# Optimization experiments

Measured on AMD Instinct MI355X. Metric: run time of the kernel, lower is better.

## Reference

```python
import jax, jax.numpy as jnp
import numpy as np


def setup_inputs() -> dict:
    B, K, E, M, H, T, V = 32, 64, 512, 512, 512, 20, 32000
    key = jax.random.key(0)
    ks = jax.random.split(key, 8)
    s = 0.02
    return {
        "encoder_outputs": jax.random.normal(ks[0], (B, K, E), jnp.float32),
        "embedding_table": jax.random.normal(ks[1], (V, M), jnp.float32) * s,
        "Wa": jax.random.normal(ks[2], (2 * H + E, 1), jnp.float32) * s,
        "ba": jnp.zeros((1,), jnp.float32),
        "W_ih": jax.random.normal(ks[3], (4 * H, E + M), jnp.float32) * s,
        "W_hh": jax.random.normal(ks[4], (4 * H, H), jnp.float32) * s,
        "b_ih": jnp.zeros((4 * H,), jnp.float32),
        "b_hh": jnp.zeros((4 * H,), jnp.float32),
        "Wl": jax.random.normal(ks[5], (V, 2 * H + E + M), jnp.float32) * s,
        "bl": jnp.zeros((V,), jnp.float32),
        "captions": jax.random.randint(ks[6], (B, T), 0, V),
        "use_teacher_forcing": 1,
    }


def reference(encoder_outputs, embedding_table, Wa, ba, W_ih, W_hh, b_ih, b_hh,
              Wl, bl, captions, use_teacher_forcing):
    B, K, E = encoder_outputs.shape
    H = W_hh.shape[1]
    tf = bool(use_teacher_forcing)  # static python flag

    # h0 = c0 = last encoder output (requires E == H, as in the source)
    h0 = encoder_outputs[:, -1, :]
    c0 = h0

    caps_seq = captions.T  # (T, B); captions[:, i] becomes next token after step i

    def step(carry, cap_t):
        h, c, token = carry
        emb = embedding_table[token]                       # (B, M), dropout=0
        flat_state = jnp.concatenate([h, c], axis=-1)      # (B, 2H)
        # Bahdanau alignment over all K encoder steps at once
        al_in = jnp.concatenate(
            [jnp.broadcast_to(flat_state[:, None, :], (B, K, 2 * H)),
             encoder_outputs], axis=-1)                    # (B, K, 2H+E)
        scores = jnp.tanh(al_in @ Wa + ba)[..., 0]         # (B, K)
        attn = jax.nn.softmax(scores, axis=1)
        context = jnp.einsum('bk,bke->be', attn, encoder_outputs)  # (B, E)
        x = jnp.concatenate([context, emb], axis=-1)       # (B, E+M) == rnn_input
        # single LSTM step, PyTorch gate order i,f,g,o
        gates = x @ W_ih.T + b_ih + h @ W_hh.T + b_hh
        i_g, f_g, g_g, o_g = jnp.split(gates, 4, axis=-1)
        c_new = jax.nn.sigmoid(f_g) * c + jax.nn.sigmoid(i_g) * jnp.tanh(g_g)
        h_new = jax.nn.sigmoid(o_g) * jnp.tanh(c_new)
        # NOTE: source concatenates the PRE-update state here (faithful)
        final_input = jnp.concatenate([flat_state, x], axis=-1)  # (B, 2H+E+M)
        logp = jax.nn.log_softmax(final_input @ Wl.T + bl, axis=1)  # (B, V)
        next_token = cap_t if tf else jnp.argmax(logp, axis=1)
        return (h_new, c_new, next_token), logp

    init = (h0, c0, captions[:, 0])
    _, probs = jax.lax.scan(step, init, caps_seq)
    return jnp.transpose(probs, (1, 0, 2))  # (B, T, V)
```

## Files before the change

### kernel.cpp

```cpp
#include <hip/hip_runtime.h>
#include <hip/hip_bf16.h>
#include <stdint.h>

#define B_   32
#define K_   64
#define E_   512
#define H_   512
#define M_   512
#define T_   20
#define V_   32000
#define KIN  2048
#define NBLK 32

typedef __bf16 bf16x8 __attribute__((ext_vector_type(8)));
typedef float  f32x4  __attribute__((ext_vector_type(4)));

__device__ inline unsigned short f2bf_rne(float f) {
  union { float f; unsigned u; } v; v.f = f;
  unsigned r = v.u + 0x7FFFu + ((v.u >> 16) & 1u);
  return (unsigned short)(r >> 16);
}
__device__ inline float bf2f(unsigned short s) {
  union { unsigned u; float f; } v; v.u = ((unsigned)s) << 16;
  return v.f;
}
__device__ inline float sigm(float x) { return 1.f / (1.f + expf(-x)); }
__device__ inline unsigned ordf(float f) {
  unsigned u = __float_as_uint(f);
  return (u & 0x80000000u) ? ~u : (u | 0x80000000u);
}
__device__ __forceinline__ void gload16(const void* g, void* l) {
  __builtin_amdgcn_global_load_lds(
      (const __attribute__((address_space(1))) void*)g,
      (__attribute__((address_space(3))) void*)l, 16, 0, 0);
}


__global__ void k_prep(const float* __restrict__ W_ih, const float* __restrict__ W_hh,
                       const float* __restrict__ b_ih, const float* __restrict__ b_hh,
                       const float* __restrict__ enc, const float* __restrict__ embt,
                       const int* __restrict__ captions,
                       unsigned short* __restrict__ wih_hi, unsigned short* __restrict__ wih_lo,
                       unsigned short* __restrict__ whh_hi, unsigned short* __restrict__ whh_lo,
                       unsigned short* __restrict__ enc_bf, unsigned short* __restrict__ emb_bf,
                       float* __restrict__ bias_arr, float* __restrict__ score_part,
                       unsigned long long* __restrict__ argkey) {
  int tid0 = blockIdx.x * 256 + threadIdx.x;
  int NT = gridDim.x * 256;
  for (int i = tid0; i < 2048 * 1024; i += NT) {
    float f = W_ih[i];
    unsigned short h = f2bf_rne(f);
    wih_hi[i] = h; wih_lo[i] = f2bf_rne(f - bf2f(h));
  }
  for (int i = tid0; i < NBLK * 64 * 512; i += NT) {
    int e = i & 511, jj = (i >> 9) & 63, blk = i >> 15;
    int jg = (jj >> 4) * 512 + blk * 16 + (jj & 15);
    float f = W_hh[jg * 512 + e];
    unsigned short h = f2bf_rne(f);
    whh_hi[i] = h; whh_lo[i] = f2bf_rne(f - bf2f(h));
  }
  for (int i = tid0; i < 2048 * 512; i += NT) enc_bf[i] = f2bf_rne(enc[i]);
  for (int i = tid0; i < 640 * 512; i += NT) {
    int n = i >> 9, m = i & 511;
    int t = n >> 5, b = n & 31;
    int tok = captions[b * T_ + (t > 0 ? t - 1 : 0)];
    emb_bf[i] = f2bf_rne(embt[(size_t)tok * 512 + m]);
  }
  for (int i = tid0; i < 2048; i += NT) {
    int blk = i >> 6, jj = i & 63;
    int jg = (jj >> 4) * 512 + blk * 16 + (jj & 15);
    bias_arr[i] = b_ih[jg] + b_hh[jg];
  }
  for (int i = tid0; i < (T_ + 1) * 1024; i += NT) score_part[i] = 0.f;
  for (int i = tid0; i < 32; i += NT) argkey[i] = 0ull;
}

__global__ void k_init(const float* __restrict__ enc, const float* __restrict__ Wa,
                       float* __restrict__ hb, float* __restrict__ cb,
                       unsigned short* __restrict__ Fall,
                       float* __restrict__ enc_score, float* __restrict__ score_part) {
  int idx = blockIdx.x * 256 + threadIdx.x;
  int b = idx >> 9, i = idx & 511;
  float v = enc[(size_t)b * K_ * E_ + (size_t)(K_ - 1) * E_ + i];
  hb[b * H_ + i] = v;
  cb[b * H_ + i] = v;
  unsigned short bv = f2bf_rne(v);
  Fall[b * KIN + i] = bv;
  Fall[b * KIN + H_ + i] = bv;
  if (idx < B_ * K_) {
    int bb = idx >> 6, k = idx & 63;
    const float4* e4  = (const float4*)(enc + ((size_t)bb * K_ + k) * E_);
    const float4* wa4 = (const float4*)(Wa + 2 * H_);
    float acc = 0.f;
    #pragma unroll 4
    for (int q = 0; q < E_ / 4; ++q) {
      float4 a = e4[q], w = wa4[q];
      acc += a.x * w.x + a.y * w.y + a.z * w.z + a.w * w.w;
    }
    enc_score[idx] = acc;
  }
  if (idx < 2048) {
    int bb = idx >> 6, l = idx & 63;
    float s = 0.f;
    #pragma unroll
    for (int q = 0; q < 8; ++q) {
      int ii = l * 8 + q;
      float hv = enc[(size_t)bb * K_ * E_ + (size_t)(K_ - 1) * E_ + ii];
      s += hv * (Wa[ii] + Wa[512 + ii]);
    }
    for (int o = 32; o; o >>= 1) s += __shfl_down(s, o);
    if (l == 0) score_part[bb] = s;
  }
}

__global__ __launch_bounds__(256) void k_gpre(
    const unsigned short* __restrict__ whi, const unsigned short* __restrict__ wlo,
    int koff, const unsigned short* __restrict__ Bm,
    float* __restrict__ outp, int N) {
  int blk = blockIdx.x, nt = blockIdx.y;
  int tid = threadIdx.x;
  int l = tid & 63, w = tid >> 6, lv = l & 15, lg = l >> 4;
  const int n0 = nt * 128 + w * 32;

  f32x4 acc[4][2];
  #pragma unroll
  for (int jf = 0; jf < 4; ++jf)
    #pragma unroll
    for (int nf = 0; nf < 2; ++nf) acc[jf][nf] = (f32x4){0.f, 0.f, 0.f, 0.f};

  #pragma unroll 4
  for (int kk = 0; kk < 16; ++kk) {
    bf16x8 bfr[2];
    #pragma unroll
    for (int nf = 0; nf < 2; ++nf)
      bfr[nf] = *(const bf16x8*)(Bm + (size_t)(n0 + nf * 16 + lv) * 512 + kk * 32 + lg * 8);
    #pragma unroll
    for (int jf = 0; jf < 4; ++jf) {
      int jg = jf * 512 + blk * 16 + lv;
      bf16x8 ahi = *(const bf16x8*)(whi + (size_t)jg * 1024 + koff + kk * 32 + lg * 8);
      bf16x8 alo = *(const bf16x8*)(wlo + (size_t)jg * 1024 + koff + kk * 32 + lg * 8);
      #pragma unroll
      for (int nf = 0; nf < 2; ++nf) {
        acc[jf][nf] = __builtin_amdgcn_mfma_f32_16x16x32_bf16(ahi, bfr[nf], acc[jf][nf], 0, 0, 0);
        acc[jf][nf] = __builtin_amdgcn_mfma_f32_16x16x32_bf16(alo, bfr[nf], acc[jf][nf], 0, 0, 0);
      }
    }
  }
  #pragma unroll
  for (int jf = 0; jf < 4; ++jf)
    #pragma unroll
    for (int nf = 0; nf < 2; ++nf)
      #pragma unroll
      for (int jr = 0; jr < 4; ++jr) {
        int n = n0 + nf * 16 + lv;
        int jj = jf * 16 + 4 * lg + jr;
        outp[((size_t)blk * N + n) * 64 + jj] = acc[jf][nf][jr];
      }
}

__global__ __launch_bounds__(256) void k_step(
    const float* __restrict__ enc, const float* __restrict__ embt,
    const float* __restrict__ Wa, const float* __restrict__ ba,
    const float* __restrict__ W_ih, const float* __restrict__ W_hh,
    const float* __restrict__ b_ih, const float* __restrict__ b_hh,
    const float* __restrict__ Wl, const float* __restrict__ bl,
    const int* __restrict__ captions, const int* __restrict__ tf_flag,
    const float* __restrict__ Genc, const float* __restrict__ Gemb,
    const unsigned short* __restrict__ whh_hi, const unsigned short* __restrict__ whh_lo,
    const float* __restrict__ bias_arr, const float* __restrict__ enc_score,
    float* __restrict__ score_part, float* __restrict__ attn_w,
    unsigned short* __restrict__ Fall, float* __restrict__ hb, float* __restrict__ cb,
    unsigned long long* __restrict__ argkey, int t) {
  const int blk = blockIdx.x;
  const int tid = threadIdx.x;
  __shared__ float attn_s[B_ * K_];
  __shared__ float gsA[64 * 33];
  __shared__ float scC[512];
  __shared__ float score_t[32];
  const float* cbc = cb + (t & 1) * B_ * H_;
  float* cbn = cb + ((t + 1) & 1) * B_ * H_;

  if (tf_flag[0]) {
    if (tid < 32) {
      float s = 0.f;
      #pragma unroll 8
      for (int p = 0; p < 32; ++p) s += score_part[t * 1024 + p * 32 + tid];
      score_t[tid] = s;
    }
    __syncthreads();
    {
      int w = tid >> 6, l = tid & 63;
      float ba0 = ba[0];
      for (int bb = 0; bb < 8; ++bb) {
        int b = w * 8 + bb;
        float s = tanhf(score_t[b] + enc_score[b * 64 + l] + ba0);
        float m = s;
        for (int o = 32; o; o >>= 1) m = fmaxf(m, __shfl_xor(m, o));
        float e = expf(s - m);
        float sum = e;
        for (int o = 32; o; o >>= 1) sum += __shfl_xor(sum, o);
        float a = e / sum;
        attn_s[b * 64 + l] = a;
        if (b == blk) attn_w[(t * 32 + b) * 64 + l] = a;
      }
    }
    __syncthreads();
    {
      const f32x4* G4 = (const f32x4*)Genc;
      const f32x4* E4 = (const f32x4*)Gemb;
      const f32x4* B4 = (const f32x4*)bias_arr;
      #pragma unroll
      for (int rr = 0; rr < 2; ++rr) {
        int idx = rr * 256 + tid;
        int b = idx >> 4, jj4 = idx & 15;
        const f32x4* gp = G4 + ((size_t)blk * 2048 + b * 64) * 16 + jj4;
        const float* ap = attn_s + b * 64;
        f32x4 s = {0.f, 0.f, 0.f, 0.f};
        #pragma unroll 8
        for (int k = 0; k < 64; ++k) {
          float a = ap[k];
          f32x4 g = gp[(size_t)k * 16];
          s[0] += a * g[0]; s[1] += a * g[1]; s[2] += a * g[2]; s[3] += a * g[3];
        }
        f32x4 e = E4[((size_t)blk * 640 + t * 32 + b) * 16 + jj4];
        f32x4 bb = B4[blk * 16 + jj4];
        #pragma unroll
        for (int q = 0; q < 4; ++q) {
          float v = s[q] + (e[q] + bb[q]);
          gsA[(jj4 * 4 + q) * 33 + b] = v;
        }
      }
    }
    __syncthreads();
    {
      int g = tid >> 6, l = tid & 63, lv = l & 15, lg = l >> 4;
      const unsigned short* ah = whh_hi + ((size_t)blk * 64 + g * 16 + lv) * 512 + lg * 8;
      const unsigned short* al = whh_lo + ((size_t)blk * 64 + g * 16 + lv) * 512 + lg * 8;
      const unsigned short* f0 = Fall + ((size_t)t * 32 + lv) * KIN + lg * 8;
      const unsigned short* f1 = Fall + ((size_t)t * 32 + 16 + lv) * KIN + lg * 8;
      f32x4 a0 = {0.f, 0.f, 0.f, 0.f};
      f32x4 a1 = {0.f, 0.f, 0.f, 0.f};
      #pragma unroll 8
      for (int kk = 0; kk < 16; ++kk) {
        bf16x8 hi = *(const bf16x8*)(ah + kk * 32);
        bf16x8 lo = *(const bf16x8*)(al + kk * 32);
        bf16x8 b0 = *(const bf16x8*)(f0 + kk * 32);
        bf16x8 b1 = *(const bf16x8*)(f1 + kk * 32);
        a0 = __builtin_amdgcn_mfma_f32_16x16x32_bf16(hi, b0, a0, 0, 0, 0);
        a0 = __builtin_amdgcn_mfma_f32_16x16x32_bf16(lo, b0, a0, 0, 0, 0);
        a1 = __builtin_amdgcn_mfma_f32_16x16x32_bf16(hi, b1, a1, 0, 0, 0);
        a1 = __builtin_amdgcn_mfma_f32_16x16x32_bf16(lo, b1, a1, 0, 0, 0);
      }
      #pragma unroll
      for (int jr = 0; jr < 4; ++jr) {
        int jj = g * 16 + 4 * lg + jr;
        gsA[jj * 33 + lv]      += a0[jr];
        gsA[jj * 33 + 16 + lv] += a1[jr];
      }
    }
    __syncthreads();
    #pragma unroll
    for (int rr = 0; rr < 2; ++rr) {
      int idx = tid + rr * 256;
      int b = idx & 31, r = idx >> 5;
      int ii = blk * 16 + r;
      float ig = gsA[(r) * 33 + b];
      float fg = gsA[(16 + r) * 33 + b];
      float gg = gsA[(32 + r) * 33 + b];
      float og = gsA[(48 + r) * 33 + b];
      float cv = cbc[b * H_ + ii];
      float cn = sigm(fg) * cv + sigm(ig) * tanhf(gg);
      float hn = sigm(og) * tanhf(cn);
      cbn[b * H_ + ii] = cn;
      Fall[((size_t)(t + 1) * 32 + b) * KIN + ii] = f2bf_rne(hn);
      Fall[((size_t)(t + 1) * 32 + b) * KIN + H_ + ii] = f2bf_rne(cn);
      scC[r * 32 + b] = hn * Wa[ii] + cn * Wa[512 + ii];
    }
    __syncthreads();
    if (tid < 32) {
      float s = 0.f;
      #pragma unroll
      for (int r = 0; r < 16; ++r) s += scC[r * 32 + tid];
      score_part[(t + 1) * 1024 + blk * 32 + tid] = s;
    }
  } else {
    const int b = blk;
    __shared__ float xls[KIN];
    __shared__ float gls[2048];
    __shared__ int tok_s;
    __shared__ unsigned long long bred[256];
    const float* hbc = hb + (t & 1) * B_ * H_;
    float* hbn = hb + ((t + 1) & 1) * B_ * H_;
    if (tid == 0) {
      float s = 0.f;
      for (int p = 0; p < 32; ++p) s += score_part[t * 1024 + p * 32 + b];
      score_t[0] = s;
      tok_s = (t == 0) ? captions[b * T_]
                       : (int)(0xFFFFFFFFu - (unsigned)(argkey[b] & 0xFFFFFFFFull));
    }
    __syncthreads();
    if (tid < 64) {
      float s = tanhf(score_t[0] + enc_score[b * 64 + tid] + ba[0]);
      float m = s;
      for (int o = 32; o; o >>= 1) m = fmaxf(m, __shfl_xor(m, o));
      float e = expf(s - m);
      float sum = e;
      for (int o = 32; o; o >>= 1) sum += __shfl_xor(sum, o);
      attn_s[tid] = e / sum;
    }
    __syncthreads();
    for (int i = tid; i < 512; i += 256) {
      xls[i] = hbc[b * H_ + i];
      xls[512 + i] = cbc[b * H_ + i];
      float a = 0.f;
      for (int k = 0; k < 64; ++k) a += attn_s[k] * enc[((size_t)b * 64 + k) * 512 + i];
      xls[1024 + i] = a;
      xls[1536 + i] = embt[(size_t)tok_s * 512 + i];
    }
    __syncthreads();
    for (int i = tid; i < 1024; i += 256)
      Fall[((size_t)t * 32 + b) * KIN + 1024 + i] = f2bf_rne(xls[1024 + i]);
    for (int j = tid; j < 2048; j += 256) {
      float a = b_ih[j] + b_hh[j];
      for (int e = 0; e < 1024; ++e) a += W_ih[(size_t)j * 1024 + e] * xls[1024 + e];
      for (int e = 0; e < 512; ++e)  a += W_hh[(size_t)j * 512 + e] * xls[e];
      gls[j] = a;
    }
    __syncthreads();
    {
      float sc = 0.f;
      for (int i = tid; i < 512; i += 256) {
        float ig = gls[i], fg = gls[512 + i], gg = gls[1024 + i], og = gls[1536 + i];
        float cv = xls[512 + i];
        float cn = sigm(fg) * cv + sigm(ig) * tanhf(gg);
        float hn = sigm(og) * tanhf(cn);
        hbn[b * H_ + i] = hn;
        cbn[b * H_ + i] = cn;
        Fall[((size_t)(t + 1) * 32 + b) * KIN + i] = f2bf_rne(hn);
        Fall[((size_t)(t + 1) * 32 + b) * KIN + H_ + i] = f2bf_rne(cn);
        sc += hn * Wa[i] + cn * Wa[512 + i];
      }
      scC[tid] = sc;
    }
    __syncthreads();
    if (tid == 0) {
      float s = 0.f;
      for (int q = 0; q < 256; ++q) s += scC[q];
      score_part[(t + 1) * 1024 + b] = s;
    }
    unsigned long long best = 0ull;
    for (int v = tid; v < V_; v += 256) {
      float d = bl[v];
      const float* wr = Wl + (size_t)v * KIN;
      for (int k = 0; k < KIN; ++k) d += wr[k] * xls[k];
      unsigned long long key = ((unsigned long long)ordf(d) << 32) | (0xFFFFFFFFu - (unsigned)v);
      if (key > best) best = key;
    }
    bred[tid] = best;
    __syncthreads();
    for (int o = 128; o; o >>= 1) {
      if (tid < o) bred[tid] = bred[tid] > bred[tid + o] ? bred[tid] : bred[tid + o];
      __syncthreads();
    }
    if (tid == 0) argkey[b] = bred[0];
  }
}

__global__ void k_fill(const float* __restrict__ enc, const unsigned short* __restrict__ emb_bf,
                       const float* __restrict__ attn_w, const int* __restrict__ tf_flag,
                       unsigned short* __restrict__ Fall) {
  if (tf_flag[0] == 0) return;
  int n = blockIdx.x;
  int b = n & 31;
  int tid = threadIdx.x;
  __shared__ float aw[64];
  if (tid < 64) aw[tid] = attn_w[n * 64 + tid];
  __syncthreads();
  for (int e = tid; e < 512; e += 256) {
    float a = 0.f;
    #pragma unroll 8
    for (int k = 0; k < 64; ++k) a += aw[k] * enc[((size_t)b * 64 + k) * 512 + e];
    Fall[(size_t)n * KIN + 1024 + e] = f2bf_rne(a);
  }
  for (int m = tid; m < 512; m += 256)
    Fall[(size_t)n * KIN + 1536 + m] = emb_bf[n * 512 + m];
}

__global__ void k_conv(const float* __restrict__ src, unsigned short* __restrict__ dst, int n4) {
  int i = blockIdx.x * blockDim.x + threadIdx.x;
  int stride = gridDim.x * blockDim.x;
  for (; i < n4; i += stride) {
    f32x4 v = __builtin_nontemporal_load((const f32x4*)src + i);
    ushort4 o;
    o.x = f2bf_rne(v.x); o.y = f2bf_rne(v.y); o.z = f2bf_rne(v.z); o.w = f2bf_rne(v.w);
    ((ushort4*)dst)[i] = o;
  }
}

#define GM   128
#define GNP  320
#define ABYTES 40960
#define BUFB  57344

__global__ __launch_bounds__(512, 2) void k_gemm(
    const unsigned short* __restrict__ wl_bf,
    const unsigned short* __restrict__ F,
    const float* __restrict__ bl,
    float* __restrict__ out) {
  extern __shared__ unsigned char lds[];
  const int tid = threadIdx.x;
  const int l = tid & 63, w = tid >> 6, lv = l & 15, lg = l >> 4;
  const int wm = w >> 2, wn = w & 3;
  const int m0 = blockIdx.x * GM;

  float blv[4];
  #pragma unroll
  for (int mi = 0; mi < 4; ++mi) blv[mi] = bl[m0 + wm * 64 + mi * 16 + lv];

  f32x4 acc[4][5];
  #pragma unroll
  for (int mi = 0; mi < 4; ++mi)
    #pragma unroll
    for (int ni = 0; ni < 5; ++ni) acc[mi][ni] = (f32x4){0.f, 0.f, 0.f, 0.f};

#define STAGE(c, buf) do {                                                    \
    int kb_ = ((c) & 31) * 64;                                                \
    int nb_ = ((c) >> 5) * GNP;                                               \
    unsigned char* bs_ = lds + (buf) * BUFB;                                  \
    _Pragma("unroll")                                                         \
    for (int i_ = 0; i_ < 5; ++i_) {                                          \
      int s_ = i_ * 512 + tid;                                                \
      int kq_ = s_ / 320, n_ = s_ - kq_ * 320;                                \
      gload16(F + (size_t)(nb_ + n_) * KIN + kb_ + kq_ * 8, bs_ + s_ * 16);   \
    }                                                                         \
    _Pragma("unroll")                                                         \
    for (int j_ = 0; j_ < 2; ++j_) {                                          \
      int s_ = j_ * 512 + tid;                                                \
      int kq_ = s_ >> 7, m_ = s_ & 127;                                       \
      gload16(wl_bf + (size_t)(m0 + m_) * KIN + kb_ + kq_ * 8,                \
              bs_ + ABYTES + s_ * 16);                                        \
    }                                                                         \
  } while (0)

#define COMPUTE(buf) do {                                                     \
    unsigned char* bs_ = lds + (buf) * BUFB;                                  \
    _Pragma("unroll")                                                         \
    for (int kk2_ = 0; kk2_ < 2; ++kk2_) {                                    \
      int kq_ = kk2_ * 4 + lg;                                                \
      bf16x8 bf_[4];                                                          \
      _Pragma("unroll")                                                       \
      for (int mi = 0; mi < 4; ++mi)                                          \
        bf_[mi] = *(const bf16x8*)(bs_ + ABYTES +                             \
                    (size_t)(kq_ * 128 + wm * 64 + mi * 16 + lv) * 16);       \
      _Pragma("unroll")                                                       \
      for (int ni = 0; ni < 5; ++ni) {                                        \
        bf16x8 af_ = *(const bf16x8*)(bs_ +                                   \
                    (size_t)(kq_ * 320 + wn * 80 + ni * 16 + lv) * 16);       \
        _Pragma("unroll")                                                     \
        for (int mi = 0; mi < 4; ++mi)                                        \
          acc[mi][ni] = __builtin_amdgcn_mfma_f32_16x16x32_bf16(              \
                          af_, bf_[mi], acc[mi][ni], 0, 0, 0);                \
      }                                                                       \
    }                                                                         \
  } while (0)

#define WRITEOUT(pass) do {                                                   \
    _Pragma("unroll")                                                         \
    for (int mi = 0; mi < 4; ++mi) {                                          \
      int v_ = m0 + wm * 64 + mi * 16 + lv;                                   \
      _Pragma("unroll")                                                       \
      for (int ni = 0; ni < 5; ++ni) {                                        \
        _Pragma("unroll")                                                     \
        for (int j_ = 0; j_ < 4; ++j_) {                                      \
          int n_ = (pass) * GNP + wn * 80 + ni * 16 + 4 * lg + j_;            \
          int tt_ = n_ >> 5, bb_ = n_ & 31;                                   \
          out[((size_t)bb_ * T_ + tt_) * V_ + v_] = acc[mi][ni][j_] + blv[mi];\
        }                                                                     \
      }                                                                       \
    }                                                                         \
  } while (0)

  STAGE(0, 0);
  int cur = 0;
  for (int c = 0; c < 64; ++c) {
    __syncthreads();
    if (c < 63) STAGE(c + 1, cur ^ 1);
    COMPUTE(cur);
    if (c == 31) {
      WRITEOUT(0);
      #pragma unroll
      for (int mi = 0; mi < 4; ++mi)
        #pragma unroll
        for (int ni = 0; ni < 5; ++ni) acc[mi][ni] = (f32x4){0.f, 0.f, 0.f, 0.f};
    }
    cur ^= 1;
  }
  WRITEOUT(1);
#undef STAGE
#undef COMPUTE
#undef WRITEOUT
}

__global__ void k_lsm(float* __restrict__ out) {
  float4* p = (float4*)(out + (size_t)blockIdx.x * V_);
  int tid = threadIdx.x;
  __shared__ float smax[4], ssum[4];
  const int N4 = V_ / 4;
  float m = -1e30f, s = 0.f;
  for (int i = tid; i < N4; i += 256) {
    float4 v = p[i];
    float lm = fmaxf(fmaxf(v.x, v.y), fmaxf(v.z, v.w));
    if (lm > m) { s *= expf(m - lm); m = lm; }
    s += expf(v.x - m) + expf(v.y - m) + expf(v.z - m) + expf(v.w - m);
  }
  for (int o = 32; o; o >>= 1) {
    float m2 = __shfl_xor(m, o), s2 = __shfl_xor(s, o);
    float mn = fmaxf(m, m2);
    s = s * expf(m - mn) + s2 * expf(m2 - mn);
    m = mn;
  }
  if ((tid & 63) == 0) { smax[tid >> 6] = m; ssum[tid >> 6] = s; }
  __syncthreads();
  float mg = fmaxf(fmaxf(smax[0], smax[1]), fmaxf(smax[2], smax[3]));
  float sg = ssum[0] * expf(smax[0] - mg) + ssum[1] * expf(smax[1] - mg)
           + ssum[2] * expf(smax[2] - mg) + ssum[3] * expf(smax[3] - mg);
  float lse = mg + logf(sg);
  for (int i = tid; i < N4; i += 256) {
    float4 v = p[i];
    v.x -= lse; v.y -= lse; v.z -= lse; v.w -= lse;
    p[i] = v;
  }
}

extern "C" void kernel_launch(void* const* d_in, const int* in_sizes, int n_in,
                              void* d_out, int out_size, void* d_ws, size_t ws_size,
                              hipStream_t stream) {
  const float* enc      = (const float*)d_in[0];
  const float* embt     = (const float*)d_in[1];
  const float* Wa       = (const float*)d_in[2];
  const float* ba       = (const float*)d_in[3];
  const float* W_ih     = (const float*)d_in[4];
  const float* W_hh     = (const float*)d_in[5];
  const float* b_ih     = (const float*)d_in[6];
  const float* b_hh     = (const float*)d_in[7];
  const float* Wl       = (const float*)d_in[8];
  const float* bl       = (const float*)d_in[9];
  const int*   captions = (const int*)d_in[10];
  const int*   tf       = (const int*)d_in[11];
  float* out = (float*)d_out;
  char*  ws  = (char*)d_ws;

  size_t off = 0;
  unsigned short* Fall = (unsigned short*)(ws + off); off += (size_t)(T_ + 1) * B_ * KIN * 2;
  float* hb            = (float*)(ws + off);          off += (size_t)2 * B_ * H_ * 4;
  float* cb            = (float*)(ws + off);          off += (size_t)2 * B_ * H_ * 4;
  float* enc_score     = (float*)(ws + off);          off += (size_t)B_ * K_ * 4;
  float* score_part    = (float*)(ws + off);          off += (size_t)(T_ + 1) * 1024 * 4;
  float* attn_w        = (float*)(ws + off);          off += (size_t)T_ * B_ * K_ * 4;
  unsigned long long* argkey = (unsigned long long*)(ws + off); off += 256;
  float* bias_arr      = (float*)(ws + off);          off += 2048 * 4;
  off = (off + 1023) & ~(size_t)1023;
  unsigned short* wih_hi = (unsigned short*)(ws + off); off += (size_t)2048 * 1024 * 2;
  unsigned short* wih_lo = (unsigned short*)(ws + off); off += (size_t)2048 * 1024 * 2;
  unsigned short* whh_hi = (unsigned short*)(ws + off); off += (size_t)NBLK * 64 * 512 * 2;
  unsigned short* whh_lo = (unsigned short*)(ws + off); off += (size_t)NBLK * 64 * 512 * 2;
  unsigned short* enc_bf = (unsigned short*)(ws + off); off += (size_t)2048 * 512 * 2;
  unsigned short* emb_bf = (unsigned short*)(ws + off); off += (size_t)640 * 512 * 2;
  float* Genc          = (float*)(ws + off);          off += (size_t)NBLK * 2048 * 64 * 4;
  float* Gemb          = (float*)(ws + off);          off += (size_t)NBLK * 640 * 64 * 4;
  unsigned short* wl_bf = (unsigned short*)(ws + off); off += (size_t)V_ * KIN * 2;

  k_prep<<<512, 256, 0, stream>>>(W_ih, W_hh, b_ih, b_hh, enc, embt, captions,
                                  wih_hi, wih_lo, whh_hi, whh_lo, enc_bf, emb_bf,
                                  bias_arr, score_part, argkey);
  k_init<<<64, 256, 0, stream>>>(enc, Wa, hb, cb, Fall, enc_score, score_part);
  k_gpre<<<dim3(NBLK, 16), 256, 0, stream>>>(wih_hi, wih_lo, 0, enc_bf, Genc, 2048);
  k_gpre<<<dim3(NBLK, 5), 256, 0, stream>>>(wih_hi, wih_lo, 512, emb_bf, Gemb, 640);

  for (int t = 0; t < T_; ++t) {
    k_step<<<NBLK, 256, 0, stream>>>(enc, embt, Wa, ba, W_ih, W_hh, b_ih, b_hh,
                                     Wl, bl, captions, tf, Genc, Gemb,
                                     whh_hi, whh_lo, bias_arr, enc_score,
                                     score_part, attn_w, Fall, hb, cb, argkey, t);
  }
  k_fill<<<T_ * B_, 256, 0, stream>>>(enc, emb_bf, attn_w, tf, Fall);
  k_conv<<<8192, 256, 0, stream>>>(Wl, wl_bf, V_ * KIN / 4);
  k_gemm<<<V_ / GM, 512, 2 * BUFB, stream>>>(wl_bf, Fall, bl, out);
  k_lsm<<<B_ * T_, 256, 0, stream>>>(out);
}
```

Before: 813.4 us.

## Fuse per-step launches into one cooperative kernel and fold fill/conv into prep

Replaces the 20 per-timestep k_step launches with a single cooperative kernel that loops over timesteps and uses grid.sync between steps. The context-vector write to Fall now happens inside the step loop, removing k_fill and the attn_w buffer. The Wl-to-bf16 conversion and the embedding copy into Fall move into k_prep, removing the separate k_conv launch. This trades per-launch overhead for grid-wide barrier cost, and makes k_prep heavier.

```diff
diff --git a/kernel.cpp b/kernel.cpp
--- a/kernel.cpp
+++ b/kernel.cpp
@@ -1,6 +1,9 @@
 #include <hip/hip_runtime.h>
 #include <hip/hip_bf16.h>
+#include <hip/hip_cooperative_groups.h>
 #include <stdint.h>
+
+namespace cg = cooperative_groups;
 
 #define B_   32
 #define K_   64
@@ -44,9 +47,17 @@
                        unsigned short* __restrict__ whh_hi, unsigned short* __restrict__ whh_lo,
                        unsigned short* __restrict__ enc_bf, unsigned short* __restrict__ emb_bf,
                        float* __restrict__ bias_arr, float* __restrict__ score_part,
-                       unsigned long long* __restrict__ argkey) {
+                       unsigned long long* __restrict__ argkey,
+                       const float* __restrict__ Wl, unsigned short* __restrict__ wl_bf,
+                       unsigned short* __restrict__ Fall) {
   int tid0 = blockIdx.x * 256 + threadIdx.x;
   int NT = gridDim.x * 256;
+  for (int i = tid0; i < V_ * KIN / 4; i += NT) {
+    f32x4 v = __builtin_nontemporal_load((const f32x4*)Wl + i);
+    ushort4 o;
+    o.x = f2bf_rne(v.x); o.y = f2bf_rne(v.y); o.z = f2bf_rne(v.z); o.w = f2bf_rne(v.w);
+    ((ushort4*)wl_bf)[i] = o;
+  }
   for (int i = tid0; i < 2048 * 1024; i += NT) {
     float f = W_ih[i];
     unsigned short h = f2bf_rne(f);
@@ -64,7 +75,9 @@
     int n = i >> 9, m = i & 511;
     int t = n >> 5, b = n & 31;
     int tok = captions[b * T_ + (t > 0 ? t - 1 : 0)];
-    emb_bf[i] = f2bf_rne(embt[(size_t)tok * 512 + m]);
+    unsigned short ev = f2bf_rne(embt[(size_t)tok * 512 + m]);
+    emb_bf[i] = ev;
+    Fall[(size_t)n * KIN + 1536 + m] = ev;
   }
   for (int i = tid0; i < 2048; i += NT) {
     int blk = i >> 6, jj = i & 63;
@@ -158,7 +171,7 @@
       }
 }
 
-__global__ __launch_bounds__(256) void k_step(
+__global__ __launch_bounds__(256) void k_chain(
     const float* __restrict__ enc, const float* __restrict__ embt,
     const float* __restrict__ Wa, const float* __restrict__ ba,
     const float* __restrict__ W_ih, const float* __restrict__ W_hh,
@@ -168,232 +181,214 @@
     const float* __restrict__ Genc, const float* __restrict__ Gemb,
     const unsigned short* __restrict__ whh_hi, const unsigned short* __restrict__ whh_lo,
     const float* __restrict__ bias_arr, const float* __restrict__ enc_score,
-    float* __restrict__ score_part, float* __restrict__ attn_w,
-    unsigned short* __restrict__ Fall, float* __restrict__ hb, float* __restrict__ cb,
-    unsigned long long* __restrict__ argkey, int t) {
+    float* __restrict__ score_part, unsigned short* __restrict__ Fall,
+    float* __restrict__ hb, float* __restrict__ cb,
+    unsigned long long* __restrict__ argkey) {
+  cg::grid_group grid = cg::this_grid();
   const int blk = blockIdx.x;
   const int tid = threadIdx.x;
   __shared__ float attn_s[B_ * K_];
   __shared__ float gsA[64 * 33];
   __shared__ float scC[512];
-  __shared__ float score_t[32];
-  const float* cbc = cb + (t & 1) * B_ * H_;
-  float* cbn = cb + ((t + 1) & 1) * B_ * H_;
-
-  if (tf_flag[0]) {
-    if (tid < 32) {
-      float s = 0.f;
-      #pragma unroll 8
-      for (int p = 0; p < 32; ++p) s += score_part[t * 1024 + p * 32 + tid];
-      score_t[tid] = s;
-    }
-    __syncthreads();
-    {
-      int w = tid >> 6, l = tid & 63;
-      float ba0 = ba[0];
-      for (int bb = 0; bb < 8; ++bb) {
-        int b = w * 8 + bb;
-        float s = tanhf(score_t[b] + enc_score[b * 64 + l] + ba0);
+  __shared__ float score_t_[32];
+  __shared__ int   token_sp;
+  __shared__ float xls[KIN];
+  __shared__ float gls[2048];
+  __shared__ unsigned long long bred[256];
+  const int tf = tf_flag[0];
+
+  for (int t = 0; t < T_; ++t) {
+    const float* cbc = cb + (t & 1) * B_ * H_;
+    float* cbn = cb + ((t + 1) & 1) * B_ * H_;
+
+    if (tf) {
+      if (tid < 32) {
+        float s = 0.f;
+        #pragma unroll 8
+        for (int p = 0; p < 32; ++p) s += score_part[t * 1024 + p * 32 + tid];
+        score_t_[tid] = s;
+      }
+      __syncthreads();
+      {
+        int w = tid >> 6, l = tid & 63;
+        float ba0 = ba[0];
+        for (int bb = 0; bb < 8; ++bb) {
+          int b = w * 8 + bb;
+          float s = tanhf(score_t_[b] + enc_score[b * 64 + l] + ba0);
+          float m = s;
+          for (int o = 32; o; o >>= 1) m = fmaxf(m, __shfl_xor(m, o));
+          float e = expf(s - m);
+          float sum = e;
+          for (int o = 32; o; o >>= 1) sum += __shfl_xor(sum, o);
+          attn_s[b * 64 + l] = e / sum;
+        }
+      }
+      __syncthreads();
+      {
+        const f32x4* G4 = (const f32x4*)Genc;
+        const f32x4* E4 = (const f32x4*)Gemb;
+        const f32x4* B4 = (const f32x4*)bias_arr;
+        #pragma unroll
+        for (int rr = 0; rr < 2; ++rr) {
+          int idx = rr * 256 + tid;
+          int b = idx >> 4, jj4 = idx & 15;
+          const f32x4* gp = G4 + ((size_t)blk * 2048 + b * 64) * 16 + jj4;
+          const float* ap = attn_s + b * 64;
+          f32x4 s = {0.f, 0.f, 0.f, 0.f};
+          #pragma unroll 8
+          for (int k = 0; k < 64; ++k) {
+            float a = ap[k];
+            f32x4 g = gp[(size_t)k * 16];
+            s[0] += a * g[0]; s[1] += a * g[1]; s[2] += a * g[2]; s[3] += a * g[3];
+          }
+          f32x4 e = E4[((size_t)blk * 640 + t * 32 + b) * 16 + jj4];
+          f32x4 bb = B4[blk * 16 + jj4];
+          #pragma unroll
+          for (int q = 0; q < 4; ++q) {
+            float v = s[q] + (e[q] + bb[q]);
+            gsA[(jj4 * 4 + q) * 33 + b] = v;
+          }
+        }
+      }
+      {
+        const float* aw = attn_s + blk * 64;
+        for (int e = tid; e < 512; e += 256) {
+          float a = 0.f;
+          #pragma unroll 8
+          for (int k = 0; k < 64; ++k) a += aw[k] * enc[((size_t)blk * 64 + k) * 512 + e];
+          Fall[((size_t)t * 32 + blk) * KIN + 1024 + e] = f2bf_rne(a);
+        }
+      }
+      __syncthreads();
+      {
+        int g = tid >> 6, l = tid & 63, lv = l & 15, lg = l >> 4;
+        const unsigned short* ah = whh_hi + ((size_t)blk * 64 + g * 16 + lv) * 512 + lg * 8;
+        const unsigned short* al = whh_lo + ((size_t)blk * 64 + g * 16 + lv) * 512 + lg * 8;
+        const unsigned short* f0 = Fall + ((size_t)t * 32 + lv) * KIN + lg * 8;
+        const unsigned short* f1 = Fall + ((size_t)t * 32 + 16 + lv) * KIN + lg * 8;
+        f32x4 a0 = {0.f, 0.f, 0.f, 0.f};
+        f32x4 a1 = {0.f, 0.f, 0.f, 0.f};
+        #pragma unroll 8
+        for (int kk = 0; kk < 16; ++kk) {
+          bf16x8 hi = *(const bf16x8*)(ah + kk * 32);
+          bf16x8 lo = *(const bf16x8*)(al + kk * 32);
+          bf16x8 b0 = *(const bf16x8*)(f0 + kk * 32);
+          bf16x8 b1 = *(const bf16x8*)(f1 + kk * 32);
+          a0 = __builtin_amdgcn_mfma_f32_16x16x32_bf16(hi, b0, a0, 0, 0, 0);
+          a0 = __builtin_amdgcn_mfma_f32_16x16x32_bf16(lo, b0, a0, 0, 0, 0);
+          a1 = __builtin_amdgcn_mfma_f32_16x16x32_bf16(hi, b1, a1, 0, 0, 0);
+          a1 = __builtin_amdgcn_mfma_f32_16x16x32_bf16(lo, b1, a1, 0, 0, 0);
+        }
+        #pragma unroll
+        for (int jr = 0; jr < 4; ++jr) {
+          int jj = g * 16 + 4 * lg + jr;
+          gsA[jj * 33 + lv]      += a0[jr];
+          gsA[jj * 33 + 16 + lv] += a1[jr];
+        }
+      }
+      __syncthreads();
+      #pragma unroll
+      for (int rr = 0; rr < 2; ++rr) {
+        int idx = tid + rr * 256;
+        int b = idx & 31, r = idx >> 5;
+        int ii = blk * 16 + r;
+        float ig = gsA[(r) * 33 + b];
+        float fg = gsA[(16 + r) * 33 + b];
+        float gg = gsA[(32 + r) * 33 + b];
+        float og = gsA[(48 + r) * 33 + b];
+        float cv = cbc[b * H_ + ii];
+        float cn = sigm(fg) * cv + sigm(ig) * tanhf(gg);
+        float hn = sigm(og) * tanhf(cn);
+        cbn[b * H_ + ii] = cn;
+        Fall[((size_t)(t + 1) * 32 + b) * KIN + ii] = f2bf_rne(hn);
+        Fall[((size_t)(t + 1) * 32 + b) * KIN + H_ + ii] = f2bf_rne(cn);
+        scC[r * 32 + b] = hn * Wa[ii] + cn * Wa[512 + ii];
+      }
+      __syncthreads();
+      if (tid < 32) {
+        float s = 0.f;
+        #pragma unroll
+        for (int r = 0; r < 16; ++r) s += scC[r * 32 + tid];
+        score_part[(t + 1) * 1024 + blk * 32 + tid] = s;
+      }
+    } else {
+      const int b = blk;
+      const float* hbc = hb + (t & 1) * B_ * H_;
+      float* hbn = hb + ((t + 1) & 1) * B_ * H_;
+      if (tid == 0) {
+        float s = 0.f;
+        for (int p = 0; p < 32; ++p) s += score_part[t * 1024 + p * 32 + b];
+        score_t_[0] = s;
+        token_sp = (t == 0) ? captions[b * T_]
+                            : (int)(0xFFFFFFFFu - (unsigned)(argkey[b] & 0xFFFFFFFFull));
+      }
+      __syncthreads();
+      if (tid < 64) {
+        float s = tanhf(score_t_[0] + enc_score[b * 64 + tid] + ba[0]);
         float m = s;
         for (int o = 32; o; o >>= 1) m = fmaxf(m, __shfl_xor(m, o));
         float e = expf(s - m);
         float sum = e;
         for (int o = 32; o; o >>= 1) sum += __shfl_xor(sum, o);
-        float a = e / sum;
-        attn_s[b * 64 + l] = a;
-        if (b == blk) attn_w[(t * 32 + b) * 64 + l] = a;
-      }
+        attn_s[tid] = e / sum;
+      }
+      __syncthreads();
+      for (int i = tid; i < 512; i += 256) {
+        xls[i] = hbc[b * H_ + i];
+        xls[512 + i] = cbc[b * H_ + i];
+        float a = 0.f;
+        for (int k = 0; k < 64; ++k) a += attn_s[k] * enc[((size_t)b * 64 + k) * 512 + i];
+        xls[1024 + i] = a;
+        xls[1536 + i] = embt[(size_t)token_sp * 512 + i];
+      }
+      __syncthreads();
+      for (int i = tid; i < 1024; i += 256)
+        Fall[((size_t)t * 32 + b) * KIN + 1024 + i] = f2bf_rne(xls[1024 + i]);
+      for (int j = tid; j < 2048; j += 256) {
+        float a = b_ih[j] + b_hh[j];
+        for (int e = 0; e < 1024; ++e) a += W_ih[(size_t)j * 1024 + e] * xls[1024 + e];
+        for (int e = 0; e < 512; ++e)  a += W_hh[(size_t)j * 512 + e] * xls[e];
+        gls[j] = a;
+      }
+      __syncthreads();
+      {
+        float sc = 0.f;
+        for (int i = tid; i < 512; i += 256) {
+          float ig = gls[i], fg = gls[512 + i], gg = gls[1024 + i], og = gls[1536 + i];
+          float cv = xls[512 + i];
+          float cn = sigm(fg) * cv + sigm(ig) * tanhf(gg);
+          float hn = sigm(og) * tanhf(cn);
+          hbn[b * H_ + i] = hn;
+          cbn[b * H_ + i] = cn;
+          Fall[((size_t)(t + 1) * 32 + b) * KIN + i] = f2bf_rne(hn);
+          Fall[((size_t)(t + 1) * 32 + b) * KIN + H_ + i] = f2bf_rne(cn);
+          sc += hn * Wa[i] + cn * Wa[512 + i];
+        }
+        scC[tid] = sc;
+      }
+      __syncthreads();
+      if (tid == 0) {
+        float s = 0.f;
+        for (int q = 0; q < 256; ++q) s += scC[q];
+        score_part[(t + 1) * 1024 + b] = s;
+      }
+      unsigned long long best = 0ull;
+      for (int v = tid; v < V_; v += 256) {
+        float d = bl[v];
+        const float* wr = Wl + (size_t)v * KIN;
+        for (int k = 0; k < KIN; ++k) d += wr[k] * xls[k];
+        unsigned long long key = ((unsigned long long)ordf(d) << 32) | (0xFFFFFFFFu - (unsigned)v);
+        if (key > best) best = key;
+      }
+      bred[tid] = best;
+      __syncthreads();
+      for (int o = 128; o; o >>= 1) {
+        if (tid < o) bred[tid] = bred[tid] > bred[tid + o] ? bred[tid] : bred[tid + o];
+        __syncthreads();
+      }
+      if (tid == 0) argkey[b] = bred[0];
     }
-    __syncthreads();
-    {
-      const f32x4* G4 = (const f32x4*)Genc;
-      const f32x4* E4 = (const f32x4*)Gemb;
-      const f32x4* B4 = (const f32x4*)bias_arr;
-      #pragma unroll
-      for (int rr = 0; rr < 2; ++rr) {
-        int idx = rr * 256 + tid;
-        int b = idx >> 4, jj4 = idx & 15;
-        const f32x4* gp = G4 + ((size_t)blk * 2048 + b * 64) * 16 + jj4;
-        const float* ap = attn_s + b * 64;
-        f32x4 s = {0.f, 0.f, 0.f, 0.f};
-        #pragma unroll 8
-        for (int k = 0; k < 64; ++k) {
-          float a = ap[k];
-          f32x4 g = gp[(size_t)k * 16];
-          s[0] += a * g[0]; s[1] += a * g[1]; s[2] += a * g[2]; s[3] += a * g[3];
-        }
-        f32x4 e = E4[((size_t)blk * 640 + t * 32 + b) * 16 + jj4];
-        f32x4 bb = B4[blk * 16 + jj4];
-        #pragma unroll
-        for (int q = 0; q < 4; ++q) {
-          float v = s[q] + (e[q] + bb[q]);
-          gsA[(jj4 * 4 + q) * 33 + b] = v;
-        }
-      }
-    }
-    __syncthreads();
-    {
-      int g = tid >> 6, l = tid & 63, lv = l & 15, lg = l >> 4;
-      const unsigned short* ah = whh_hi + ((size_t)blk * 64 + g * 16 + lv) * 512 + lg * 8;
-      const unsigned short* al = whh_lo + ((size_t)blk * 64 + g * 16 + lv) * 512 + lg * 8;
-      const unsigned short* f0 = Fall + ((size_t)t * 32 + lv) * KIN + lg * 8;
-      const unsigned short* f1 = Fall + ((size_t)t * 32 + 16 + lv) * KIN + lg * 8;
-      f32x4 a0 = {0.f, 0.f, 0.f, 0.f};
-      f32x4 a1 = {0.f, 0.f, 0.f, 0.f};
-      #pragma unroll 8
-      for (int kk = 0; kk < 16; ++kk) {
-        bf16x8 hi = *(const bf16x8*)(ah + kk * 32);
-        bf16x8 lo = *(const bf16x8*)(al + kk * 32);
-        bf16x8 b0 = *(const bf16x8*)(f0 + kk * 32);
-        bf16x8 b1 = *(const bf16x8*)(f1 + kk * 32);
-        a0 = __builtin_amdgcn_mfma_f32_16x16x32_bf16(hi, b0, a0, 0, 0, 0);
-        a0 = __builtin_amdgcn_mfma_f32_16x16x32_bf16(lo, b0, a0, 0, 0, 0);
-        a1 = __builtin_amdgcn_mfma_f32_16x16x32_bf16(hi, b1, a1, 0, 0, 0);
-        a1 = __builtin_amdgcn_mfma_f32_16x16x32_bf16(lo, b1, a1, 0, 0, 0);
-      }
-      #pragma unroll
-      for (int jr = 0; jr < 4; ++jr) {
-        int jj = g * 16 + 4 * lg + jr;
-        gsA[jj * 33 + lv]      += a0[jr];
-        gsA[jj * 33 + 16 + lv] += a1[jr];
-      }
-    }
-    __syncthreads();
-    #pragma unroll
-    for (int rr = 0; rr < 2; ++rr) {
-      int idx = tid + rr * 256;
-      int b = idx & 31, r = idx >> 5;
-      int ii = blk * 16 + r;
-      float ig = gsA[(r) * 33 + b];
-      float fg = gsA[(16 + r) * 33 + b];
-      float gg = gsA[(32 + r) * 33 + b];
-      float og = gsA[(48 + r) * 33 + b];
-      float cv = cbc[b * H_ + ii];
-      float cn = sigm(fg) * cv + sigm(ig) * tanhf(gg);
-      float hn = sigm(og) * tanhf(cn);
-      cbn[b * H_ + ii] = cn;
-      Fall[((size_t)(t + 1) * 32 + b) * KIN + ii] = f2bf_rne(hn);
-      Fall[((size_t)(t + 1) * 32 + b) * KIN + H_ + ii] = f2bf_rne(cn);
-      scC[r * 32 + b] = hn * Wa[ii] + cn * Wa[512 + ii];
-    }
-    __syncthreads();
-    if (tid < 32) {
-      float s = 0.f;
-      #pragma unroll
-      for (int r = 0; r < 16; ++r) s += scC[r * 32 + tid];
-      score_part[(t + 1) * 1024 + blk * 32 + tid] = s;
-    }
-  } else {
-    const int b = blk;
-    __shared__ float xls[KIN];
-    __shared__ float gls[2048];
-    __shared__ int tok_s;
-    __shared__ unsigned long long bred[256];
-    const float* hbc = hb + (t & 1) * B_ * H_;
-    float* hbn = hb + ((t + 1) & 1) * B_ * H_;
-    if (tid == 0) {
-      float s = 0.f;
-      for (int p = 0; p < 32; ++p) s += score_part[t * 1024 + p * 32 + b];
-      score_t[0] = s;
-      tok_s = (t == 0) ? captions[b * T_]
-                       : (int)(0xFFFFFFFFu - (unsigned)(argkey[b] & 0xFFFFFFFFull));
-    }
-    __syncthreads();
-    if (tid < 64) {
-      float s = tanhf(score_t[0] + enc_score[b * 64 + tid] + ba[0]);
-      float m = s;
-      for (int o = 32; o; o >>= 1) m = fmaxf(m, __shfl_xor(m, o));
-      float e = expf(s - m);
-      float sum = e;
-      for (int o = 32; o; o >>= 1) sum += __shfl_xor(sum, o);
-      attn_s[tid] = e / sum;
-    }
-    __syncthreads();
-    for (int i = tid; i < 512; i += 256) {
-      xls[i] = hbc[b * H_ + i];
-      xls[512 + i] = cbc[b * H_ + i];
-      float a = 0.f;
-      for (int k = 0; k < 64; ++k) a += attn_s[k] * enc[((size_t)b * 64 + k) * 512 + i];
-      xls[1024 + i] = a;
-      xls[1536 + i] = embt[(size_t)tok_s * 512 + i];
-    }
-    __syncthreads();
-    for (int i = tid; i < 1024; i += 256)
-      Fall[((size_t)t * 32 + b) * KIN + 1024 + i] = f2bf_rne(xls[1024 + i]);
-    for (int j = tid; j < 2048; j += 256) {
-      float a = b_ih[j] + b_hh[j];
-      for (int e = 0; e < 1024; ++e) a += W_ih[(size_t)j * 1024 + e] * xls[1024 + e];
-      for (int e = 0; e < 512; ++e)  a += W_hh[(size_t)j * 512 + e] * xls[e];
-      gls[j] = a;
-    }
-    __syncthreads();
-    {
-      float sc = 0.f;
-      for (int i = tid; i < 512; i += 256) {
-        float ig = gls[i], fg = gls[512 + i], gg = gls[1024 + i], og = gls[1536 + i];
-        float cv = xls[512 + i];
-        float cn = sigm(fg) * cv + sigm(ig) * tanhf(gg);
-        float hn = sigm(og) * tanhf(cn);
-        hbn[b * H_ + i] = hn;
-        cbn[b * H_ + i] = cn;
-        Fall[((size_t)(t + 1) * 32 + b) * KIN + i] = f2bf_rne(hn);
-        Fall[((size_t)(t + 1) * 32 + b) * KIN + H_ + i] = f2bf_rne(cn);
-        sc += hn * Wa[i] + cn * Wa[512 + i];
-      }
-      scC[tid] = sc;
-    }
-    __syncthreads();
-    if (tid == 0) {
-      float s = 0.f;
-      for (int q = 0; q < 256; ++q) s += scC[q];
-      score_part[(t + 1) * 1024 + b] = s;
-    }
-    unsigned long long best = 0ull;
-    for (int v = tid; v < V_; v += 256) {
-      float d = bl[v];
-      const float* wr = Wl + (size_t)v * KIN;
-      for (int k = 0; k < KIN; ++k) d += wr[k] * xls[k];
-      unsigned long long key = ((unsigned long long)ordf(d) << 32) | (0xFFFFFFFFu - (unsigned)v);
-      if (key > best) best = key;
-    }
-    bred[tid] = best;
-    __syncthreads();
-    for (int o = 128; o; o >>= 1) {
-      if (tid < o) bred[tid] = bred[tid] > bred[tid + o] ? bred[tid] : bred[tid + o];
-      __syncthreads();
-    }
-    if (tid == 0) argkey[b] = bred[0];
-  }
-}
-
-__global__ void k_fill(const float* __restrict__ enc, const unsigned short* __restrict__ emb_bf,
-                       const float* __restrict__ attn_w, const int* __restrict__ tf_flag,
-                       unsigned short* __restrict__ Fall) {
-  if (tf_flag[0] == 0) return;
-  int n = blockIdx.x;
-  int b = n & 31;
-  int tid = threadIdx.x;
-  __shared__ float aw[64];
-  if (tid < 64) aw[tid] = attn_w[n * 64 + tid];
-  __syncthreads();
-  for (int e = tid; e < 512; e += 256) {
-    float a = 0.f;
-    #pragma unroll 8
-    for (int k = 0; k < 64; ++k) a += aw[k] * enc[((size_t)b * 64 + k) * 512 + e];
-    Fall[(size_t)n * KIN + 1024 + e] = f2bf_rne(a);
-  }
-  for (int m = tid; m < 512; m += 256)
-    Fall[(size_t)n * KIN + 1536 + m] = emb_bf[n * 512 + m];
-}
-
-__global__ void k_conv(const float* __restrict__ src, unsigned short* __restrict__ dst, int n4) {
-  int i = blockIdx.x * blockDim.x + threadIdx.x;
-  int stride = gridDim.x * blockDim.x;
-  for (; i < n4; i += stride) {
-    f32x4 v = __builtin_nontemporal_load((const f32x4*)src + i);
-    ushort4 o;
-    o.x = f2bf_rne(v.x); o.y = f2bf_rne(v.y); o.z = f2bf_rne(v.z); o.w = f2bf_rne(v.w);
-    ((ushort4*)dst)[i] = o;
+    grid.sync();
   }
 }
 
@@ -556,7 +551,6 @@
   float* cb            = (float*)(ws + off);          off += (size_t)2 * B_ * H_ * 4;
   float* enc_score     = (float*)(ws + off);          off += (size_t)B_ * K_ * 4;
   float* score_part    = (float*)(ws + off);          off += (size_t)(T_ + 1) * 1024 * 4;
-  float* attn_w        = (float*)(ws + off);          off += (size_t)T_ * B_ * K_ * 4;
   unsigned long long* argkey = (unsigned long long*)(ws + off); off += 256;
   float* bias_arr      = (float*)(ws + off);          off += 2048 * 4;
   off = (off + 1023) & ~(size_t)1023;
@@ -572,19 +566,24 @@
 
   k_prep<<<512, 256, 0, stream>>>(W_ih, W_hh, b_ih, b_hh, enc, embt, captions,
                                   wih_hi, wih_lo, whh_hi, whh_lo, enc_bf, emb_bf,
-                                  bias_arr, score_part, argkey);
+                                  bias_arr, score_part, argkey, Wl, wl_bf, Fall);
   k_init<<<64, 256, 0, stream>>>(enc, Wa, hb, cb, Fall, enc_score, score_part);
   k_gpre<<<dim3(NBLK, 16), 256, 0, stream>>>(wih_hi, wih_lo, 0, enc_bf, Genc, 2048);
   k_gpre<<<dim3(NBLK, 5), 256, 0, stream>>>(wih_hi, wih_lo, 512, emb_bf, Gemb, 640);
 
-  for (int t = 0; t < T_; ++t) {
-    k_step<<<NBLK, 256, 0, stream>>>(enc, embt, Wa, ba, W_ih, W_hh, b_ih, b_hh,
-                                     Wl, bl, captions, tf, Genc, Gemb,
-                                     whh_hi, whh_lo, bias_arr, enc_score,
-                                     score_part, attn_w, Fall, hb, cb, argkey, t);
-  }
-  k_fill<<<T_ * B_, 256, 0, stream>>>(enc, emb_bf, attn_w, tf, Fall);
-  k_conv<<<8192, 256, 0, stream>>>(Wl, wl_bf, V_ * KIN / 4);
+  {
+    void* args[] = {
+      (void*)&enc, (void*)&embt, (void*)&Wa, (void*)&ba,
+      (void*)&W_ih, (void*)&W_hh, (void*)&b_ih, (void*)&b_hh,
+      (void*)&Wl, (void*)&bl, (void*)&captions, (void*)&tf,
+      (void*)&Genc, (void*)&Gemb, (void*)&whh_hi, (void*)&whh_lo,
+      (void*)&bias_arr, (void*)&enc_score, (void*)&score_part, (void*)&Fall,
+      (void*)&hb, (void*)&cb, (void*)&argkey
+    };
+    hipLaunchCooperativeKernel((void*)k_chain, dim3(NBLK), dim3(256),
+                               args, 0, stream);
+  }
+
   k_gemm<<<V_ / GM, 512, 2 * BUFB, stream>>>(wl_bf, Fall, bl, out);
   k_lsm<<<B_ * T_, 256, 0, stream>>>(out);
 }
```

Result: slower. 994.2 us (+22.2%).
